# Performance work log

Hardware: AMD Instinct MI355X
Metric: run time of the kernel (lower is better)

Reference implementation:

```python
import jax, jax.numpy as jnp
import numpy as np

B, N, D_IN = 8, 2048, 512
H = 1024          # MLP hidden
D_EMB = 512       # embed output dim
D_ATTN = 256      # attn_layers[-1]; KQ MLP outputs 2*D_ATTN


def setup_inputs() -> dict:
    key = jax.random.key(0)
    ks = jax.random.split(key, 9)
    s = lambda fi, fo: (2.0 / (fi + fo)) ** 0.5
    return {
        "x": jax.random.normal(ks[0], (B, N, D_IN), dtype=jnp.float32),
        # embed MLP: Linear(D_IN,H), ReLU, Linear(H,D_EMB)  (weights stored [in,out])
        "We1": jax.random.normal(ks[1], (D_IN, H), dtype=jnp.float32) * s(D_IN, H),
        "be1": jnp.zeros((H,), dtype=jnp.float32),
        "We2": jax.random.normal(ks[2], (H, D_EMB), dtype=jnp.float32) * s(H, D_EMB),
        "be2": jnp.zeros((D_EMB,), dtype=jnp.float32),
        # KQ MLP: Linear(D_IN,H), ReLU, Linear(H, 2*D_ATTN)
        "Wk1": jax.random.normal(ks[3], (D_IN, H), dtype=jnp.float32) * s(D_IN, H),
        "bk1": jnp.zeros((H,), dtype=jnp.float32),
        "Wk2": jax.random.normal(ks[4], (H, 2 * D_ATTN), dtype=jnp.float32) * s(H, 2 * D_ATTN),
        "bk2": jnp.zeros((2 * D_ATTN,), dtype=jnp.float32),
    }


def reference(x, We1, be1, We2, be2, Wk1, bk1, Wk2, bk2):
    # embed MLP
    embs = jax.nn.relu(x @ We1 + be1) @ We2 + be2            # [B,N,D_EMB]
    # KQ MLP; chunk: first half K, second half Q
    kq = jax.nn.relu(x @ Wk1 + bk1) @ Wk2 + bk2              # [B,N,2*D_ATTN]
    K, Q = kq[..., :D_ATTN], kq[..., D_ATTN:]
    # unscaled attention: softmax(Q K^T) V
    scores = jnp.einsum("bqd,bkd->bqk", Q, K)                # [B,N,N]
    A = jax.nn.softmax(scores, axis=-1)
    return jnp.einsum("bqk,bkd->bqd", A, embs)               # [B,N,D_EMB]
```

## Files before the change

kernel.cpp:

```cpp
#include <hip/hip_runtime.h>
#include <stdint.h>

using fx4   = __attribute__((ext_vector_type(4))) float;
using half8 = __attribute__((ext_vector_type(8))) _Float16;

__device__ __forceinline__ ushort f2h(float x) {
  _Float16 h = (_Float16)x;
  union { _Float16 hv; ushort u; } v; v.hv = h;
  return v.u;
}

__device__ __forceinline__ void gload_lds16(const ushort* g, ushort* l) {
  __builtin_amdgcn_global_load_lds(
      (__attribute__((address_space(1))) const void*)g,
      (__attribute__((address_space(3))) void*)l, 16, 0, 0);
}

#define MFMA16(a, b, c) __builtin_amdgcn_mfma_f32_16x16x32_f16(a, b, c, 0, 0, 0)

__device__ __forceinline__ void gemm_body(
    const ushort* __restrict__ A, int lda,
    const ushort* __restrict__ B, int ldb,
    const float* __restrict__ bias,
    void* __restrict__ C, int ldc,
    int K, int flags, int bx, int by,
    ushort* As, ushort* Bs, ushort* __restrict__ C2 = nullptr)
{
  const int tid  = threadIdx.x;
  const int lane = tid & 63;
  const int wave = tid >> 6;
  const int wm   = (wave >> 1) * 64;
  const int wn   = (wave & 1) * 64;
  const long long bm = (long long)by * 128;
  const long long bn = (long long)bx * 128;

  const int srow = tid >> 2;
  const int skq  = (tid & 3) * 8;
  const ushort* a0 = A + (bm + srow) * lda + skq;
  const ushort* a1 = a0 + 64LL * lda;
  const ushort* b0 = B + (bn + srow) * ldb + skq;
  const ushort* b1 = b0 + 64LL * ldb;
  ushort* lA0 = &As[tid * 8];
  ushort* lA1 = &As[2048 + tid * 8];
  ushort* lB0 = &Bs[tid * 8];
  ushort* lB1 = &Bs[2048 + tid * 8];

  fx4 acc[4][4] = {};
  const ushort* ap = &As[(wm + (lane & 15)) * 32 + (lane >> 4) * 8];
  const ushort* bp = &Bs[(wn + (lane & 15)) * 32 + (lane >> 4) * 8];

  for (int k0 = 0; k0 < K; k0 += 32) {
    gload_lds16(a0, lA0);
    gload_lds16(a1, lA1);
    gload_lds16(b0, lB0);
    gload_lds16(b1, lB1);
    a0 += 32; a1 += 32; b0 += 32; b1 += 32;
    __syncthreads();
    half8 af[4], bv[4];
#pragma unroll
    for (int t = 0; t < 4; ++t) {
      af[t] = *(const half8*)(ap + t * 16 * 32);
      bv[t] = *(const half8*)(bp + t * 16 * 32);
    }
#pragma unroll
    for (int i = 0; i < 4; ++i)
#pragma unroll
      for (int j = 0; j < 4; ++j)
        acc[i][j] = MFMA16(af[i], bv[j], acc[i][j]);
    __syncthreads();
  }

  const int col0 = (int)bn + wn + (lane & 15);
  const int row0 = (int)bm + wm + ((lane >> 4) << 2);

  if (flags & 16) {
    ushort* Ch = (ushort*)C;
#pragma unroll
    for (int j = 0; j < 4; ++j) {
      const int col = col0 + j * 16;
      const float bvv = bias ? bias[col] : 0.0f;
#pragma unroll
      for (int i = 0; i < 4; ++i) {
        const int row = row0 + i * 16;
        ushort4 o;
        o.x = f2h(acc[i][j][0] + bvv);
        o.y = f2h(acc[i][j][1] + bvv);
        o.z = f2h(acc[i][j][2] + bvv);
        o.w = f2h(acc[i][j][3] + bvv);
        *(ushort4*)(Ch + (long long)(row >> 5) * 16384 + (long long)col * 32 + (row & 31)) = o;
      }
    }
    return;
  }

  if (flags & 32) {
    ushort* KTp = (ushort*)C;
#pragma unroll
    for (int j = 0; j < 4; ++j) {
      const int col = col0 + j * 16;
      const float bvv = bias ? bias[col] : 0.0f;
#pragma unroll
      for (int i = 0; i < 4; ++i) {
        const int row = row0 + i * 16;
#pragma unroll
        for (int r = 0; r < 4; ++r) {
          const float v = acc[i][j][r] + bvv;
          if (col < 256) {
            const int tok = row + r;
            KTp[(long long)(tok >> 5) * 8192 + (col >> 5) * 1024 +
                (tok & 31) * 32 + (col & 31)] = f2h(v);
          } else {
            C2[(long long)(row + r) * 256 + (col - 256)] = f2h(v);
          }
        }
      }
    }
    return;
  }

  float*  Cf = (float*)C;
  ushort* Ch = (ushort*)C;
#pragma unroll
  for (int j = 0; j < 4; ++j) {
    const int col = col0 + j * 16;
    const float bvv = bias ? bias[col] : 0.0f;
#pragma unroll
    for (int i = 0; i < 4; ++i) {
      const long long row = row0 + i * 16;
#pragma unroll
      for (int r = 0; r < 4; ++r) {
        float v = acc[i][j][r] + bvv;
        if (flags & 1) v = fmaxf(v, 0.0f);
        if (flags & 2) Ch[(row + r) * ldc + col] = f2h(v);
        else           Cf[(row + r) * ldc + col] = v;
      }
    }
  }
}

__global__ __launch_bounds__(256)
void gemm_bt(const ushort* __restrict__ A, int lda, long long sA,
             const ushort* __restrict__ B, int ldb, long long sB,
             const float* __restrict__ bias,
             void* __restrict__ C, int ldc, long long sC,
             int K, int flags)
{
  __shared__ ushort As[128 * 32];
  __shared__ ushort Bs[128 * 32];
  const int z = blockIdx.z;
  void* Cz = (flags & 2) ? (void*)((ushort*)C + (long long)z * sC)
                         : (void*)((float*)C + (long long)z * sC);
  gemm_body(A + (long long)z * sA, lda, B + (long long)z * sB, ldb, bias,
            Cz, ldc, K, flags, blockIdx.x, blockIdx.y, As, Bs);
}

__global__ __launch_bounds__(256)
void gemm2_pair(const ushort* __restrict__ H, const ushort* __restrict__ W2c,
                const float* __restrict__ be2, const float* __restrict__ bk2,
                ushort* __restrict__ VT, ushort* __restrict__ KT,
                ushort* __restrict__ Qm)
{
  __shared__ ushort As[128 * 32];
  __shared__ ushort Bs[128 * 32];
  if (blockIdx.z == 0)
    gemm_body(H, 2048, W2c, 1024, be2, VT, 0, 1024, 16,
              blockIdx.x, blockIdx.y, As, Bs);
  else
    gemm_body(H + 1024, 2048, W2c + 524288, 1024, bk2, KT, 0, 1024, 32,
              blockIdx.x, blockIdx.y, As, Bs, Qm);
}

__global__ __launch_bounds__(512, 2)
void attn_fused(const ushort* __restrict__ KT, const ushort* __restrict__ VT,
                const ushort* __restrict__ Qm, float* __restrict__ out)
{
  __shared__ ushort Qs[20480];
  __shared__ ushort Ps[10240];
  __shared__ float  rmax[256];
  __shared__ float  alphaA[64];
  __shared__ float  lred[256];

  const int tid  = threadIdx.x;
  const int lane = tid & 63;
  const int w    = tid >> 6;
  const int c    = lane & 15;
  const int q4   = lane >> 4;
  const int qw   = w >> 2;
  const int tw   = w & 3;
  const int dw   = w * 64;
  const int z    = blockIdx.x;
  const long long tb = (long long)z * 2048;
  const long long pbase = (long long)z * 64;
  const int q0   = blockIdx.y * 64;

#pragma unroll
  for (int p = 0; p < 4; ++p) {
    const int cu  = p * 512 + tid;
    const int row = cu >> 5;
    const int kch = cu & 31;
    const int dc  = kch >> 2, qg = kch & 3;
    const half8 v = *(const half8*)(Qm + (tb + q0 + row) * 256 + dc * 32 + qg * 8);
    *(half8*)(Qs + dc * 2560 + row * 40 + qg * 8) = v;
  }
  __syncthreads();

  float m_reg[2][4], l_part[2][4];
#pragma unroll
  for (int i = 0; i < 2; ++i)
#pragma unroll
    for (int r = 0; r < 4; ++r) { m_reg[i][r] = -3.0e38f; l_part[i][r] = 0.0f; }
  fx4 o[4][4] = {};

  for (int t0 = 0; t0 < 2048; t0 += 128) {
    const long long pt = pbase + (t0 >> 5);
    half8 kb[2][8];
    const ushort* kp = KT + (pt + tw) * 8192;
#pragma unroll
    for (int dc = 0; dc < 8; ++dc) {
      kb[0][dc] = *(const half8*)(kp + dc * 1024 + c * 32 + q4 * 8);
      kb[1][dc] = *(const half8*)(kp + dc * 1024 + (16 + c) * 32 + q4 * 8);
    }
    fx4 s[2][2] = {};
#pragma unroll
    for (int dc = 0; dc < 8; ++dc) {
      const half8 a0 = *(const half8*)(Qs + dc * 2560 + (qw * 32 + c) * 40 + q4 * 8);
      const half8 a1 = *(const half8*)(Qs + dc * 2560 + (qw * 32 + 16 + c) * 40 + q4 * 8);
      s[0][0] = MFMA16(a0, kb[0][dc], s[0][0]); s[0][1] = MFMA16(a0, kb[1][dc], s[0][1]);
      s[1][0] = MFMA16(a1, kb[0][dc], s[1][0]); s[1][1] = MFMA16(a1, kb[1][dc], s[1][1]);
    }
    half8 vb[4][4];
#pragma unroll
    for (int kc = 0; kc < 4; ++kc)
#pragma unroll
      for (int n = 0; n < 4; ++n)
        vb[kc][n] = *(const half8*)(VT + (pt + kc) * 16384 +
                                    (dw + n * 16 + c) * 32 + q4 * 8);
#pragma unroll
    for (int i = 0; i < 2; ++i) {
      fx4 rm;
#pragma unroll
      for (int r = 0; r < 4; ++r) rm[r] = fmaxf(s[i][0][r], s[i][1][r]);
#pragma unroll
      for (int off = 1; off < 16; off <<= 1)
#pragma unroll
        for (int r = 0; r < 4; ++r) rm[r] = fmaxf(rm[r], __shfl_xor(rm[r], off, 64));
      if (c == 0) {
#pragma unroll
        for (int r = 0; r < 4; ++r)
          rmax[tw * 64 + qw * 32 + i * 16 + q4 * 4 + r] = rm[r];
      }
    }
    __syncthreads();
#pragma unroll
    for (int i = 0; i < 2; ++i)
#pragma unroll
      for (int r = 0; r < 4; ++r) {
        const int q = qw * 32 + i * 16 + q4 * 4 + r;
        const float mo = m_reg[i][r];
        float mn = fmaxf(fmaxf(rmax[q], rmax[64 + q]),
                         fmaxf(rmax[128 + q], rmax[192 + q]));
        mn = fmaxf(mn, mo);
        m_reg[i][r] = mn;
        const float a  = __expf(mo - mn);
        const float e0 = __expf(s[i][0][r] - mn);
        const float e1 = __expf(s[i][1][r] - mn);
        l_part[i][r] = a * l_part[i][r] + e0 + e1;
        Ps[tw * 2560 + q * 40 + c]      = f2h(e0);
        Ps[tw * 2560 + q * 40 + 16 + c] = f2h(e1);
        if (tw == 0 && c == 0) alphaA[q] = a;
      }
    __syncthreads();
#pragma unroll
    for (int i4 = 0; i4 < 4; ++i4)
#pragma unroll
      for (int r = 0; r < 4; ++r) {
        const float aq = alphaA[i4 * 16 + q4 * 4 + r];
#pragma unroll
        for (int n = 0; n < 4; ++n) o[i4][n][r] *= aq;
      }
#pragma unroll
    for (int kc = 0; kc < 4; ++kc) {
      half8 pa[4];
#pragma unroll
      for (int i4 = 0; i4 < 4; ++i4)
        pa[i4] = *(const half8*)(Ps + kc * 2560 + (i4 * 16 + c) * 40 + q4 * 8);
#pragma unroll
      for (int i4 = 0; i4 < 4; ++i4)
#pragma unroll
        for (int n = 0; n < 4; ++n)
          o[i4][n] = MFMA16(pa[i4], vb[kc][n], o[i4][n]);
    }
  }

#pragma unroll
  for (int i = 0; i < 2; ++i) {
    fx4 lv;
#pragma unroll
    for (int r = 0; r < 4; ++r) lv[r] = l_part[i][r];
#pragma unroll
    for (int off = 1; off < 16; off <<= 1)
#pragma unroll
      for (int r = 0; r < 4; ++r) lv[r] += __shfl_xor(lv[r], off, 64);
    if (c == 0) {
#pragma unroll
      for (int r = 0; r < 4; ++r)
        lred[tw * 64 + qw * 32 + i * 16 + q4 * 4 + r] = lv[r];
    }
  }
  __syncthreads();

  float* ob = out + (tb + q0) * 512 + dw;
#pragma unroll
  for (int i4 = 0; i4 < 4; ++i4)
#pragma unroll
    for (int r = 0; r < 4; ++r) {
      const int q = i4 * 16 + q4 * 4 + r;
      const float li = 1.0f / (lred[q] + lred[64 + q] + lred[128 + q] + lred[192 + q]);
#pragma unroll
      for (int n = 0; n < 4; ++n)
        ob[(long long)q * 512 + n * 16 + c] = o[i4][n][r] * li;
    }
}

__global__ __launch_bounds__(256)
void transpose_cast_w2(const float* __restrict__ in0, const float* __restrict__ in1,
                       ushort* __restrict__ out0, ushort* __restrict__ out1,
                       int R, int C) {
  __shared__ float tile[32][33];
  const float* in  = blockIdx.z ? in1 : in0;
  ushort*      outp = blockIdx.z ? out1 : out0;
  const int c0 = blockIdx.x * 32, r0 = blockIdx.y * 32;
  const int tx = threadIdx.x & 31, ty = threadIdx.x >> 5;
#pragma unroll
  for (int i = 0; i < 32; i += 8)
    tile[ty + i][tx] = in[(long long)(r0 + ty + i) * C + (c0 + tx)];
  __syncthreads();
#pragma unroll
  for (int i = 0; i < 32; i += 8)
    outp[(long long)(c0 + ty + i) * R + (r0 + tx)] = f2h(tile[tx][ty + i]);
}

__global__ __launch_bounds__(256)
void cast_f32_f16(const float* __restrict__ in, ushort* __restrict__ out) {
  const long long i = ((long long)blockIdx.x * 256 + threadIdx.x) * 4;
  const float4 v = *(const float4*)(in + i);
  ushort4 o;
  o.x = f2h(v.x); o.y = f2h(v.y); o.z = f2h(v.z); o.w = f2h(v.w);
  *(ushort4*)(out + i) = o;
}

__global__ __launch_bounds__(256)
void concat_bias(const float* __restrict__ b0, const float* __restrict__ b1,
                 float* __restrict__ out) {
  const int i = blockIdx.x * 256 + threadIdx.x;
  out[i] = (i < 1024) ? b0[i] : b1[i - 1024];
}

extern "C" void kernel_launch(void* const* d_in, const int* in_sizes, int n_in,
                              void* d_out, int out_size, void* d_ws, size_t ws_size,
                              hipStream_t stream) {
  (void)in_sizes; (void)n_in; (void)out_size; (void)ws_size;
  const float* x   = (const float*)d_in[0];
  const float* We1 = (const float*)d_in[1];
  const float* be1 = (const float*)d_in[2];
  const float* We2 = (const float*)d_in[3];
  const float* be2 = (const float*)d_in[4];
  const float* Wk1 = (const float*)d_in[5];
  const float* bk1 = (const float*)d_in[6];
  const float* Wk2 = (const float*)d_in[7];
  const float* bk2 = (const float*)d_in[8];
  float* out = (float*)d_out;
  char* ws = (char*)d_ws;

  ushort* Xb  = (ushort*)(ws + 0);
  ushort* W2c = (ushort*)(ws + 0);
  ushort* H   = (ushort*)(ws + 16777216);
  ushort* VT  = (ushort*)(ws + 83886080);
  ushort* KT  = (ushort*)(ws + 100663296);
  ushort* Qm  = (ushort*)(ws + 109051904);
  float*  b1c = (float*)(ws + 117440512);
  ushort* W1c = (ushort*)(ws + 117448704);

  cast_f32_f16<<<dim3(8192), 256, 0, stream>>>(x, Xb);
  transpose_cast_w2<<<dim3(32, 16, 2), 256, 0, stream>>>(We1, Wk1, W1c, W1c + 524288, 512, 1024);
  concat_bias<<<dim3(8), 256, 0, stream>>>(be1, bk1, b1c);

  gemm_bt<<<dim3(16, 128, 1), 256, 0, stream>>>(Xb, 512, 0, W1c, 512, 0, b1c,
                                                H, 2048, 0, 512, 1 | 2);

  transpose_cast_w2<<<dim3(16, 32, 2), 256, 0, stream>>>(We2, Wk2, W2c, W2c + 524288, 1024, 512);

  gemm2_pair<<<dim3(4, 128, 2), 256, 0, stream>>>(H, W2c, be2, bk2, VT, KT, Qm);

  attn_fused<<<dim3(8, 32), 512, 0, stream>>>(KT, VT, Qm, out);
}
```

Before: 318.8 us.

## Double-buffer K tiles in LDS via async loads, keep Q in registers

The attention kernel now holds each wave's Q fragments in registers instead of staging Q through LDS. K tiles are streamed into a double-buffered LDS region with global_load_lds, prefetching the next 128-token tile while the current one is used. The K layout written by the second GEMM gains an XOR swizzle so the LDS fragment reads avoid bank conflicts. Dynamic shared memory grows to about 150 KB, which limits each CU to one block and raises register pressure.

```diff
diff --git a/kernel.cpp b/kernel.cpp
--- a/kernel.cpp
+++ b/kernel.cpp
@@ -107,8 +107,9 @@
           const float v = acc[i][j][r] + bvv;
           if (col < 256) {
             const int tok = row + r;
+            const int kk  = col & 31;
             KTp[(long long)(tok >> 5) * 8192 + (col >> 5) * 1024 +
-                (tok & 31) * 32 + (col & 31)] = f2h(v);
+                (tok & 31) * 32 + ((((kk >> 3) ^ (tok & 3)) << 3) | (kk & 7))] = f2h(v);
           } else {
             C2[(long long)(row + r) * 256 + (col - 256)] = f2h(v);
           }
@@ -174,11 +175,12 @@
 void attn_fused(const ushort* __restrict__ KT, const ushort* __restrict__ VT,
                 const ushort* __restrict__ Qm, float* __restrict__ out)
 {
-  __shared__ ushort Qs[20480];
-  __shared__ ushort Ps[10240];
-  __shared__ float  rmax[256];
-  __shared__ float  alphaA[64];
-  __shared__ float  lred[256];
+  extern __shared__ char smem[];
+  ushort* Kb     = (ushort*)smem;
+  ushort* Ps     = (ushort*)(smem + 131072);
+  float*  rmax   = (float*)(smem + 151552);
+  float*  alphaA = (float*)(smem + 152576);
+  float*  lred   = rmax;
 
   const int tid  = threadIdx.x;
   const int lane = tid & 63;
@@ -193,14 +195,20 @@
   const long long pbase = (long long)z * 64;
   const int q0   = blockIdx.y * 64;
 
-#pragma unroll
-  for (int p = 0; p < 4; ++p) {
-    const int cu  = p * 512 + tid;
-    const int row = cu >> 5;
-    const int kch = cu & 31;
-    const int dc  = kch >> 2, qg = kch & 3;
-    const half8 v = *(const half8*)(Qm + (tb + q0 + row) * 256 + dc * 32 + qg * 8);
-    *(half8*)(Qs + dc * 2560 + row * 40 + qg * 8) = v;
+  half8 aq[2][8];
+#pragma unroll
+  for (int i = 0; i < 2; ++i)
+#pragma unroll
+    for (int dc = 0; dc < 8; ++dc)
+      aq[i][dc] = *(const half8*)(Qm + (tb + q0 + qw * 32 + i * 16 + c) * 256 + dc * 32 + q4 * 8);
+
+  {
+    const ushort* src = KT + pbase * 8192;
+#pragma unroll
+    for (int i = 0; i < 8; ++i) {
+      const int chunk = w * 8 + i;
+      gload_lds16(src + chunk * 512 + lane * 8, Kb + chunk * 512 + lane * 8);
+    }
   }
   __syncthreads();
 
@@ -211,23 +219,11 @@
     for (int r = 0; r < 4; ++r) { m_reg[i][r] = -3.0e38f; l_part[i][r] = 0.0f; }
   fx4 o[4][4] = {};
 
+  const int swz = (q4 ^ (c & 3)) << 3;
+
+  int cur = 0;
   for (int t0 = 0; t0 < 2048; t0 += 128) {
     const long long pt = pbase + (t0 >> 5);
-    half8 kb[2][8];
-    const ushort* kp = KT + (pt + tw) * 8192;
-#pragma unroll
-    for (int dc = 0; dc < 8; ++dc) {
-      kb[0][dc] = *(const half8*)(kp + dc * 1024 + c * 32 + q4 * 8);
-      kb[1][dc] = *(const half8*)(kp + dc * 1024 + (16 + c) * 32 + q4 * 8);
-    }
-    fx4 s[2][2] = {};
-#pragma unroll
-    for (int dc = 0; dc < 8; ++dc) {
-      const half8 a0 = *(const half8*)(Qs + dc * 2560 + (qw * 32 + c) * 40 + q4 * 8);
-      const half8 a1 = *(const half8*)(Qs + dc * 2560 + (qw * 32 + 16 + c) * 40 + q4 * 8);
-      s[0][0] = MFMA16(a0, kb[0][dc], s[0][0]); s[0][1] = MFMA16(a0, kb[1][dc], s[0][1]);
-      s[1][0] = MFMA16(a1, kb[0][dc], s[1][0]); s[1][1] = MFMA16(a1, kb[1][dc], s[1][1]);
-    }
     half8 vb[4][4];
 #pragma unroll
     for (int kc = 0; kc < 4; ++kc)
@@ -235,6 +231,25 @@
       for (int n = 0; n < 4; ++n)
         vb[kc][n] = *(const half8*)(VT + (pt + kc) * 16384 +
                                     (dw + n * 16 + c) * 32 + q4 * 8);
+    {
+      const long long ptn = pbase + (((t0 + 128) & 2047) >> 5);
+      const ushort* src = KT + ptn * 8192;
+      ushort* dst = Kb + (cur ^ 1) * 32768;
+#pragma unroll
+      for (int i = 0; i < 8; ++i) {
+        const int chunk = w * 8 + i;
+        gload_lds16(src + chunk * 512 + lane * 8, dst + chunk * 512 + lane * 8);
+      }
+    }
+    const ushort* kp = Kb + cur * 32768 + tw * 8192;
+    fx4 s[2][2] = {};
+#pragma unroll
+    for (int dc = 0; dc < 8; ++dc) {
+      const half8 b0 = *(const half8*)(kp + dc * 1024 + c * 32 + swz);
+      const half8 b1 = *(const half8*)(kp + dc * 1024 + (16 + c) * 32 + swz);
+      s[0][0] = MFMA16(aq[0][dc], b0, s[0][0]); s[0][1] = MFMA16(aq[0][dc], b1, s[0][1]);
+      s[1][0] = MFMA16(aq[1][dc], b0, s[1][0]); s[1][1] = MFMA16(aq[1][dc], b1, s[1][1]);
+    }
 #pragma unroll
     for (int i = 0; i < 2; ++i) {
       fx4 rm;
@@ -274,9 +289,9 @@
     for (int i4 = 0; i4 < 4; ++i4)
 #pragma unroll
       for (int r = 0; r < 4; ++r) {
-        const float aq = alphaA[i4 * 16 + q4 * 4 + r];
-#pragma unroll
-        for (int n = 0; n < 4; ++n) o[i4][n][r] *= aq;
+        const float aq_ = alphaA[i4 * 16 + q4 * 4 + r];
+#pragma unroll
+        for (int n = 0; n < 4; ++n) o[i4][n][r] *= aq_;
       }
 #pragma unroll
     for (int kc = 0; kc < 4; ++kc) {
@@ -290,6 +305,7 @@
         for (int n = 0; n < 4; ++n)
           o[i4][n] = MFMA16(pa[i4], vb[kc][n], o[i4][n]);
     }
+    cur ^= 1;
   }
 
 #pragma unroll
@@ -392,5 +408,7 @@
 
   gemm2_pair<<<dim3(4, 128, 2), 256, 0, stream>>>(H, W2c, be2, bk2, VT, KT, Qm);
 
-  attn_fused<<<dim3(8, 32), 512, 0, stream>>>(KT, VT, Qm, out);
-}
+  hipFuncSetAttribute(reinterpret_cast<const void*>(attn_fused),
+                      hipFuncAttributeMaxDynamicSharedMemorySize, 152832);
+  attn_fused<<<dim3(8, 32), 512, 152832, stream>>>(KT, VT, Qm, out);
+}
```

After: 372.8 us. 1.17x slower.

## Split attention work across 16 waves per block instead of 8

Applied to the files above, without the earlier changes.

The fused attention kernel now runs 1024 threads per block. Each wave handles 16 key columns of the 128-key tile and 32 output dims instead of 32 keys and 64 dims. This halves per-thread accumulators and register pressure and doubles the waves available to hide latency. The cost is more cross-wave reduction in the row-max and sum steps, and the same number of barriers shared by more waves. The lred buffer now reuses the rmax storage to save LDS.

```diff
diff --git a/kernel.cpp b/kernel.cpp
--- a/kernel.cpp
+++ b/kernel.cpp
@@ -170,32 +170,32 @@
               blockIdx.x, blockIdx.y, As, Bs, Qm);
 }
 
-__global__ __launch_bounds__(512, 2)
+__global__ __launch_bounds__(1024)
 void attn_fused(const ushort* __restrict__ KT, const ushort* __restrict__ VT,
                 const ushort* __restrict__ Qm, float* __restrict__ out)
 {
   __shared__ ushort Qs[20480];
   __shared__ ushort Ps[10240];
-  __shared__ float  rmax[256];
+  __shared__ float  rmax[512];
   __shared__ float  alphaA[64];
-  __shared__ float  lred[256];
+  float* lred = rmax;
 
   const int tid  = threadIdx.x;
   const int lane = tid & 63;
   const int w    = tid >> 6;
   const int c    = lane & 15;
   const int q4   = lane >> 4;
-  const int qw   = w >> 2;
-  const int tw   = w & 3;
-  const int dw   = w * 64;
+  const int qw   = w >> 3;
+  const int tw   = w & 7;
+  const int dw   = w * 32;
   const int z    = blockIdx.x;
   const long long tb = (long long)z * 2048;
   const long long pbase = (long long)z * 64;
   const int q0   = blockIdx.y * 64;
 
 #pragma unroll
-  for (int p = 0; p < 4; ++p) {
-    const int cu  = p * 512 + tid;
+  for (int p = 0; p < 2; ++p) {
+    const int cu  = p * 1024 + tid;
     const int row = cu >> 5;
     const int kch = cu & 31;
     const int dc  = kch >> 2, qg = kch & 3;
@@ -209,37 +209,34 @@
   for (int i = 0; i < 2; ++i)
 #pragma unroll
     for (int r = 0; r < 4; ++r) { m_reg[i][r] = -3.0e38f; l_part[i][r] = 0.0f; }
-  fx4 o[4][4] = {};
+  fx4 o[4][2] = {};
 
   for (int t0 = 0; t0 < 2048; t0 += 128) {
     const long long pt = pbase + (t0 >> 5);
-    half8 kb[2][8];
-    const ushort* kp = KT + (pt + tw) * 8192;
-#pragma unroll
-    for (int dc = 0; dc < 8; ++dc) {
-      kb[0][dc] = *(const half8*)(kp + dc * 1024 + c * 32 + q4 * 8);
-      kb[1][dc] = *(const half8*)(kp + dc * 1024 + (16 + c) * 32 + q4 * 8);
-    }
-    fx4 s[2][2] = {};
+    const ushort* kp = KT + (pt + (tw >> 1)) * 8192;
+    const int toff = ((tw & 1) * 16 + c) * 32 + q4 * 8;
+    half8 kb[8];
+#pragma unroll
+    for (int dc = 0; dc < 8; ++dc)
+      kb[dc] = *(const half8*)(kp + dc * 1024 + toff);
+    fx4 s[2] = {};
 #pragma unroll
     for (int dc = 0; dc < 8; ++dc) {
       const half8 a0 = *(const half8*)(Qs + dc * 2560 + (qw * 32 + c) * 40 + q4 * 8);
       const half8 a1 = *(const half8*)(Qs + dc * 2560 + (qw * 32 + 16 + c) * 40 + q4 * 8);
-      s[0][0] = MFMA16(a0, kb[0][dc], s[0][0]); s[0][1] = MFMA16(a0, kb[1][dc], s[0][1]);
-      s[1][0] = MFMA16(a1, kb[0][dc], s[1][0]); s[1][1] = MFMA16(a1, kb[1][dc], s[1][1]);
-    }
-    half8 vb[4][4];
+      s[0] = MFMA16(a0, kb[dc], s[0]);
+      s[1] = MFMA16(a1, kb[dc], s[1]);
+    }
+    half8 vb[4][2];
 #pragma unroll
     for (int kc = 0; kc < 4; ++kc)
 #pragma unroll
-      for (int n = 0; n < 4; ++n)
+      for (int n = 0; n < 2; ++n)
         vb[kc][n] = *(const half8*)(VT + (pt + kc) * 16384 +
                                     (dw + n * 16 + c) * 32 + q4 * 8);
 #pragma unroll
     for (int i = 0; i < 2; ++i) {
-      fx4 rm;
-#pragma unroll
-      for (int r = 0; r < 4; ++r) rm[r] = fmaxf(s[i][0][r], s[i][1][r]);
+      fx4 rm = s[i];
 #pragma unroll
       for (int off = 1; off < 16; off <<= 1)
 #pragma unroll
@@ -257,16 +254,16 @@
       for (int r = 0; r < 4; ++r) {
         const int q = qw * 32 + i * 16 + q4 * 4 + r;
         const float mo = m_reg[i][r];
-        float mn = fmaxf(fmaxf(rmax[q], rmax[64 + q]),
-                         fmaxf(rmax[128 + q], rmax[192 + q]));
+        float mn = fmaxf(rmax[q], rmax[64 + q]);
+        mn = fmaxf(mn, fmaxf(rmax[128 + q], rmax[192 + q]));
+        mn = fmaxf(mn, fmaxf(rmax[256 + q], rmax[320 + q]));
+        mn = fmaxf(mn, fmaxf(rmax[384 + q], rmax[448 + q]));
         mn = fmaxf(mn, mo);
         m_reg[i][r] = mn;
-        const float a  = __expf(mo - mn);
-        const float e0 = __expf(s[i][0][r] - mn);
-        const float e1 = __expf(s[i][1][r] - mn);
-        l_part[i][r] = a * l_part[i][r] + e0 + e1;
-        Ps[tw * 2560 + q * 40 + c]      = f2h(e0);
-        Ps[tw * 2560 + q * 40 + 16 + c] = f2h(e1);
+        const float a = __expf(mo - mn);
+        const float e = __expf(s[i][r] - mn);
+        l_part[i][r] = a * l_part[i][r] + e;
+        Ps[(tw >> 1) * 2560 + q * 40 + (tw & 1) * 16 + c] = f2h(e);
         if (tw == 0 && c == 0) alphaA[q] = a;
       }
     __syncthreads();
@@ -275,8 +272,8 @@
 #pragma unroll
       for (int r = 0; r < 4; ++r) {
         const float aq = alphaA[i4 * 16 + q4 * 4 + r];
-#pragma unroll
-        for (int n = 0; n < 4; ++n) o[i4][n][r] *= aq;
+        o[i4][0][r] *= aq;
+        o[i4][1][r] *= aq;
       }
 #pragma unroll
     for (int kc = 0; kc < 4; ++kc) {
@@ -285,10 +282,10 @@
       for (int i4 = 0; i4 < 4; ++i4)
         pa[i4] = *(const half8*)(Ps + kc * 2560 + (i4 * 16 + c) * 40 + q4 * 8);
 #pragma unroll
-      for (int i4 = 0; i4 < 4; ++i4)
-#pragma unroll
-        for (int n = 0; n < 4; ++n)
-          o[i4][n] = MFMA16(pa[i4], vb[kc][n], o[i4][n]);
+      for (int i4 = 0; i4 < 4; ++i4) {
+        o[i4][0] = MFMA16(pa[i4], vb[kc][0], o[i4][0]);
+        o[i4][1] = MFMA16(pa[i4], vb[kc][1], o[i4][1]);
+      }
     }
   }
 
@@ -315,10 +312,12 @@
 #pragma unroll
     for (int r = 0; r < 4; ++r) {
       const int q = i4 * 16 + q4 * 4 + r;
-      const float li = 1.0f / (lred[q] + lred[64 + q] + lred[128 + q] + lred[192 + q]);
-#pragma unroll
-      for (int n = 0; n < 4; ++n)
-        ob[(long long)q * 512 + n * 16 + c] = o[i4][n][r] * li;
+      float ls = lred[q];
+#pragma unroll
+      for (int t = 1; t < 8; ++t) ls += lred[t * 64 + q];
+      const float li = 1.0f / ls;
+      ob[(long long)q * 512 + c]      = o[i4][0][r] * li;
+      ob[(long long)q * 512 + 16 + c] = o[i4][1][r] * li;
     }
 }
 
@@ -392,5 +391,5 @@
 
   gemm2_pair<<<dim3(4, 128, 2), 256, 0, stream>>>(H, W2c, be2, bk2, VT, KT, Qm);
 
-  attn_fused<<<dim3(8, 32), 512, 0, stream>>>(KT, VT, Qm, out);
-}
+  attn_fused<<<dim3(8, 32), 1024, 0, stream>>>(KT, VT, Qm, out);
+}
```

New measurement: 334.8 us. +5.0%, slower.
